# Performance work log

Hardware: AMD Instinct MI355X
Metric: run time of the kernel (lower is better)

The kernel has to match this reference:

```python
import jax, jax.numpy as jnp
import numpy as np

D_MODEL = 2048
D_INNER = 4096   # = d_ssm = nheads * headdim
NHEADS = 64      # = ngroups
DSTATE = 64      # = headdim (d_inner == ngroups * d_state)
D_XB = 1024      # GQA-style shared x/B width
XB_HEADS = D_XB // DSTATE    # 16
REP = NHEADS // XB_HEADS     # repeat_group = 4
DCONV = 4
CHUNK = 128
EPS = 1e-5
BATCH, SEQLEN = 1, 4096
D_IN_PROJ = 2 * D_INNER + 2 * D_XB + NHEADS  # d_mlp == 0
CONV_DIM = D_INNER + 2 * D_XB


def setup_inputs() -> dict:
    key = jax.random.key(0)
    ks = jax.random.split(key, 8)
    u = jax.random.normal(ks[0], (BATCH, SEQLEN, D_MODEL), jnp.float32)
    W_in = jax.random.normal(ks[1], (D_MODEL, D_IN_PROJ), jnp.float32) * np.float32(1.0 / np.sqrt(D_MODEL))
    conv_w = jax.random.uniform(ks[2], (CONV_DIM, DCONV), jnp.float32, -0.5, 0.5)
    conv_b = jnp.zeros((CONV_DIM,), jnp.float32)
    # dt_bias = inverse-softplus of dt sampled log-uniform in [dt_min, dt_max]
    dt = jnp.exp(jax.random.uniform(ks[3], (NHEADS,), jnp.float32) * np.float32(np.log(0.1) - np.log(0.001)) + np.float32(np.log(0.001)))
    dt = jnp.clip(dt, 1e-4, None)
    dt_bias = dt + jnp.log(-jnp.expm1(-dt))
    A_log = jnp.log(jax.random.uniform(ks[4], (NHEADS,), jnp.float32, 1.0, 16.0))
    D = jnp.ones((NHEADS,), jnp.float32)
    norm_weight = jnp.ones((D_INNER,), jnp.float32)
    W_out = jax.random.normal(ks[5], (D_INNER, D_MODEL), jnp.float32) * np.float32(1.0 / np.sqrt(D_INNER))
    return {"u": u, "W_in": W_in, "conv_w": conv_w, "conv_b": conv_b,
            "dt_bias": dt_bias, "A_log": A_log, "D": D,
            "norm_weight": norm_weight, "W_out": W_out}


def _ssd_chunked(x, dt, A, Bm, Cm):
    # x: (b,l,h,p), dt: (b,l,h) post-softplus, A: (h,) negative, Bm/Cm: (b,l,h,n)
    b, l, h, p = x.shape
    n = Bm.shape[-1]
    c, q = l // CHUNK, CHUNK
    rs = lambda t: t.reshape(b, c, q, *t.shape[2:])
    x_c, dt_c, B_c, C_c = rs(x), rs(dt), rs(Bm), rs(Cm)
    dA = dt_c * A                       # (b,c,q,h)
    cum = jnp.cumsum(dA, axis=2)        # (b,c,q,h)
    cumT = jnp.moveaxis(cum, 3, 2)      # (b,c,h,q)
    # intra-chunk: y_i += sum_{j<=i} (C_i.B_j) * exp(cum_i - cum_j) * dt_j * x_j
    diff = cumT[..., :, None] - cumT[..., None, :]               # (b,c,h,q,q)
    M = jnp.where(jnp.tril(jnp.ones((q, q), bool)), jnp.exp(diff), 0.0)
    xdt = x_c * dt_c[..., None]                                  # (b,c,q,h,p)
    G = jnp.einsum('bcihn,bcjhn->bchij', C_c, B_c)
    y = jnp.einsum('bchij,bcjhp->bcihp', G * M, xdt)
    # inter-chunk state passing
    decay_to_end = jnp.exp(cum[:, :, -1:, :] - cum)              # (b,c,q,h)
    S = jnp.einsum('bcjhn,bcjh,bcjhp->bchnp', B_c, decay_to_end, xdt)
    chunk_decay = jnp.exp(cum[:, :, -1, :])                      # (b,c,h)

    def step(H, inp):
        S_c, dec = inp
        return dec[..., None, None] * H + S_c, H

    H0 = jnp.zeros((b, h, n, p), x.dtype)
    _, Hprev = jax.lax.scan(step, H0, (jnp.moveaxis(S, 1, 0), jnp.moveaxis(chunk_decay, 1, 0)))
    Hprev = jnp.moveaxis(Hprev, 0, 1)                            # (b,c,h,n,p)
    y = y + jnp.einsum('bcihn,bcih,bchnp->bcihp', C_c, jnp.exp(cum), Hprev)
    return y.reshape(b, l, h, p)


def reference(u, W_in, conv_w, conv_b, dt_bias, A_log, D, norm_weight, W_out):
    b, l, _ = u.shape
    zxbcdt = u @ W_in                                            # (b,l,D_IN_PROJ)
    z = zxbcdt[..., :D_INNER]
    xBC = zxbcdt[..., D_INNER:D_INNER + CONV_DIM]
    dt = zxbcdt[..., D_INNER + CONV_DIM:]
    # depthwise causal conv1d + SiLU (padding d_conv-1 on the left, output len l)
    xp = jnp.pad(xBC, ((0, 0), (DCONV - 1, 0), (0, 0)))
    conv = conv_b + sum(xp[:, k:k + l, :] * conv_w[:, k] for k in range(DCONV))
    xBC = jax.nn.silu(conv)
    x = xBC[..., :D_XB]
    Bc = xBC[..., D_XB:2 * D_XB]
    Cc = xBC[..., 2 * D_XB:]
    # repeat_kv: (b,l,xb_heads,dstate) -> (b,l,nheads,dstate), interleaved repeats
    x = jnp.repeat(x.reshape(b, l, XB_HEADS, DSTATE), REP, axis=2)
    Bm = jnp.repeat(Bc.reshape(b, l, XB_HEADS, DSTATE), REP, axis=2)
    Cm = Cc.reshape(b, l, NHEADS, DSTATE)
    dt = jax.nn.softplus(dt + dt_bias)                           # dt_softplus=True
    A = -jnp.exp(A_log)
    y = _ssd_chunked(x, dt, A, Bm, Cm) + x * D[:, None]          # per-head D skip
    # gated RMSNorm: group size = d_ssm // ngroups = headdim, norm_before_gate=False
    yz = y * jax.nn.silu(z.reshape(b, l, NHEADS, DSTATE))
    normed = yz * jax.lax.rsqrt(jnp.mean(jnp.square(yz), axis=-1, keepdims=True) + EPS)
    out = normed.reshape(b, l, D_INNER) * norm_weight
    return out @ W_out
```

## Files before the change

kernel.cpp:

```cpp
#include <hip/hip_runtime.h>
#include <hip/hip_bf16.h>
#include <math.h>

typedef __hip_bfloat16 bf16;
typedef __attribute__((ext_vector_type(8))) short short8;
typedef __attribute__((ext_vector_type(4))) float f32x4;

#define D_MODEL   2048
#define D_INNER   4096
#define NHEADS    64
#define DSTATE    64
#define D_XB      1024
#define XB_HEADS  16
#define REP       4
#define DCONV     4
#define CHUNK     128
#define SEQLEN    4096
#define NCHUNK    (SEQLEN / CHUNK)
#define D_IN_PROJ (2*D_INNER + 2*D_XB + NHEADS)
#define NPAD      10496
#define CONV_DIM  (D_INNER + 2*D_XB)
#define EPS       1e-5f
#define LOG2E     1.44269504f

#define Z_BYTES    ((size_t)SEQLEN * D_INNER * 2)
#define RAW_BYTES  ((size_t)SEQLEN * CONV_DIM * 2)
#define DTP_BYTES  ((size_t)SEQLEN * NHEADS * 4)
#define CDEC_BYTES ((size_t)NCHUNK * NHEADS * 4)
#define CONV_BYTES ((size_t)SEQLEN * CONV_DIM * 2)
#define S_BYTES    ((size_t)NCHUNK * NHEADS * DSTATE * DSTATE * 4)
#define U_BYTES    ((size_t)SEQLEN * D_MODEL * 2)
#define RREG_BYTES (CONV_BYTES + S_BYTES)
#define WS_BYTES   (Z_BYTES + RAW_BYTES + DTP_BYTES + CDEC_BYTES + RREG_BYTES)

__device__ __forceinline__ short f2bf(float f) {
  bf16 h = __float2bfloat16(f);
  return *reinterpret_cast<short*>(&h);
}
__device__ __forceinline__ float bf2f(short s) {
  unsigned int u = ((unsigned int)(unsigned short)s) << 16;
  union { unsigned int u; float f; } c; c.u = u; return c.f;
}

__device__ __forceinline__ void gload_lds16(const void* g, void* l) {
  typedef __attribute__((address_space(1))) const unsigned int guint;
  typedef __attribute__((address_space(3))) unsigned int luint;
  __builtin_amdgcn_global_load_lds((guint*)g, (luint*)l, 16, 0, 0);
}

__device__ __forceinline__ char* swz128p(char* b, int r, int c) {
  int o = r * 128 + c * 2; o ^= (r & 7) << 4; return b + o;
}
__device__ __forceinline__ const char* swz128p(const char* b, int r, int c) {
  int o = r * 128 + c * 2; o ^= (r & 7) << 4; return b + o;
}
__device__ __forceinline__ char* swz256p(char* b, int r, int c) {
  int o = r * 256 + c * 2; o ^= (r & 15) << 4; return b + o;
}
__device__ __forceinline__ const char* swz256p(const char* b, int r, int c) {
  int o = r * 256 + c * 2; o ^= (r & 15) << 4; return b + o;
}

__global__ void fill_kernel(float* p, size_t n, float v) {
  size_t i = (size_t)blockIdx.x * blockDim.x + threadIdx.x;
  if (i < n) p[i] = v;
}

__global__ __launch_bounds__(256) void cast_f32_bf16(
    const float* __restrict__ in, short* __restrict__ out, size_t n4) {
  size_t i = (size_t)blockIdx.x * 256 + threadIdx.x;
  if (i >= n4) return;
  float4 v = ((const float4*)in)[i];
  short4 o;
  o.x = f2bf(v.x); o.y = f2bf(v.y); o.z = f2bf(v.z); o.w = f2bf(v.w);
  ((short4*)out)[i] = o;
}

__global__ __launch_bounds__(256) void transpose_cast(
    const float* __restrict__ in, short* __restrict__ out, int R, int C) {
  __shared__ float tile[32][130];
  const int r0 = blockIdx.y * 128;
  const int c0 = blockIdx.x * 32;
  const int tid = threadIdx.x;
  {
    int cq = tid & 7;
    int rbase = tid >> 3;
    bool valid = (c0 + cq * 4) < C;
#pragma unroll
    for (int i = 0; i < 4; ++i) {
      int r = rbase + i * 32;
      float4 v = make_float4(0.f, 0.f, 0.f, 0.f);
      if (valid) v = *(const float4*)(in + (size_t)(r0 + r) * C + c0 + cq * 4);
      tile[cq * 4 + 0][r] = v.x;
      tile[cq * 4 + 1][r] = v.y;
      tile[cq * 4 + 2][r] = v.z;
      tile[cq * 4 + 3][r] = v.w;
    }
  }
  __syncthreads();
  {
    int rq = tid & 31;
    int cbase = tid >> 5;
#pragma unroll
    for (int i = 0; i < 4; ++i) {
      int c = cbase + i * 8;
      short4 o;
      o.x = f2bf(tile[c][rq * 4 + 0]);
      o.y = f2bf(tile[c][rq * 4 + 1]);
      o.z = f2bf(tile[c][rq * 4 + 2]);
      o.w = f2bf(tile[c][rq * 4 + 3]);
      *(short4*)(out + (size_t)(c0 + c) * R + r0 + rq * 4) = o;
    }
  }
}


template<int NLOADS>
__device__ __forceinline__ void stage_half(const char* gtile, int rowbytes,
                                           char* ldst, int tid) {
#pragma unroll
  for (int i = 0; i < NLOADS; ++i) {
    int cid = i * 512 + tid;
    int r = cid >> 2;
    int pos = ((cid & 3) * 16) ^ (((r >> 1) & 3) << 4);
    gload_lds16(gtile + (size_t)r * rowbytes + pos, ldst + cid * 16);
  }
}

template<int BM>
__device__ __forceinline__ void compute_phase(const char* ldsA, const char* ldsB,
    int wm, int wn, int mh, int fr, int kqb, f32x4 (&acc)[BM / 32][4]) {
  constexpr int MF = BM / 64;
  short8 a[MF], b[4];
#pragma unroll
  for (int m = 0; m < MF; ++m) {
    int r = wm * (BM / 2) + mh * (BM / 4) + m * 16 + fr;
    a[m] = *(const short8*)(ldsA + r * 64 + (kqb ^ (((r >> 1) & 3) << 4)));
  }
#pragma unroll
  for (int n = 0; n < 4; ++n) {
    int r = wn * 64 + n * 16 + fr;
    b[n] = *(const short8*)(ldsB + r * 64 + (kqb ^ (((r >> 1) & 3) << 4)));
  }
  __builtin_amdgcn_s_setprio(1);
#pragma unroll
  for (int m = 0; m < MF; ++m)
#pragma unroll
    for (int n = 0; n < 4; ++n)
      acc[mh * MF + m][n] = __builtin_amdgcn_mfma_f32_16x16x32_bf16(a[m], b[n], acc[mh * MF + m][n], 0, 0, 0);
  __builtin_amdgcn_s_setprio(0);
}

template<int N>
__device__ __forceinline__ void wait_bar() {
  if constexpr (N == 0) asm volatile("s_waitcnt vmcnt(0)" ::: "memory");
  else if constexpr (N == 3) asm volatile("s_waitcnt vmcnt(3)" ::: "memory");
  else if constexpr (N == 4) asm volatile("s_waitcnt vmcnt(4)" ::: "memory");
  __builtin_amdgcn_s_barrier();
  __builtin_amdgcn_sched_barrier(0);
}

template<int BM>
__device__ __forceinline__ void gemm_core(const short* A, const short* Bt, int K,
    int rowBase, int colBase, char* lds, f32x4 (&acc)[BM / 32][4]) {
  constexpr int SA = BM * 64;
  constexpr int NLA = SA / 8192;
  constexpr int W = NLA + 2;
  const int tid = threadIdx.x, lane = tid & 63;
  const int w = tid >> 6, wm = w >> 2, wn = w & 3;
  const int fr = lane & 15, kqb = (lane >> 4) * 16;
  const int NT = K >> 6;
  const int rb = K * 2;
  char* ldsA = lds;
  char* ldsB = lds + 4 * SA;
  const char* Ag = (const char*)(A + (size_t)rowBase * K);
  const char* Bg = (const char*)(Bt + (size_t)colBase * K);
  stage_half<NLA>(Ag, rb, ldsA, tid);
  stage_half<2>(Bg, rb, ldsB, tid);
  stage_half<NLA>(Ag + 64, rb, ldsA + SA, tid);
  stage_half<2>(Bg + 64, rb, ldsB + 16384, tid);
  wait_bar<W>();
  for (int t = 0; t < NT; ++t) {
    const int cbA = (t & 1) * 2 * SA, nbA = ((t + 1) & 1) * 2 * SA;
    const int cbB = (t & 1) * 32768, nbB = ((t + 1) & 1) * 32768;
    const size_t ko = (size_t)(t + 1) * 128;
    const bool more = (t + 1 < NT);
    if (more) stage_half<NLA>(Ag + ko, rb, ldsA + nbA, tid);
    compute_phase<BM>(ldsA + cbA, ldsB + cbB, wm, wn, 0, fr, kqb, acc);
    if (more) stage_half<2>(Bg + ko, rb, ldsB + nbB, tid);
    compute_phase<BM>(ldsA + cbA, ldsB + cbB, wm, wn, 1, fr, kqb, acc);
    if (more) { wait_bar<W>(); } else { wait_bar<0>(); }
    if (more) stage_half<NLA>(Ag + ko + 64, rb, ldsA + nbA + SA, tid);
    compute_phase<BM>(ldsA + cbA + SA, ldsB + cbB + 16384, wm, wn, 0, fr, kqb, acc);
    if (more) stage_half<2>(Bg + ko + 64, rb, ldsB + nbB + 16384, tid);
    compute_phase<BM>(ldsA + cbA + SA, ldsB + cbB + 16384, wm, wn, 1, fr, kqb, acc);
    if (more) { wait_bar<W>(); } else { wait_bar<0>(); }
  }
}

__global__ __launch_bounds__(512) void gemm1_8ph(
    const short* __restrict__ A, const short* __restrict__ Bt,
    bf16* __restrict__ z, bf16* __restrict__ raw, float* __restrict__ dtraw) {
  __shared__ __align__(16) char lds[131072];
  f32x4 acc[8][4] = {};
  const int bid = blockIdx.x;
  const int s = (bid & 7) * 82 + (bid >> 3);
  const int rowBase = (s & 15) * 256;
  const int colBase = (s >> 4) * 256;
  gemm_core<256>(A, Bt, D_MODEL, rowBase, colBase, lds, acc);
  const int lane = threadIdx.x & 63, w = threadIdx.x >> 6;
  const int wm = w >> 2, wn = w & 3;
  const int fr = lane & 15, kq = lane >> 4;
  const int r0 = rowBase + wm * 128 + kq * 4;
  const int c0 = colBase + wn * 64 + fr;
#pragma unroll
  for (int M = 0; M < 8; ++M)
#pragma unroll
    for (int n = 0; n < 4; ++n) {
      int col = c0 + n * 16;
#pragma unroll
      for (int j = 0; j < 4; ++j) {
        int row = r0 + M * 16 + j;
        float v = acc[M][n][j];
        if (col < D_INNER) {
          z[(size_t)row * D_INNER + col] = __float2bfloat16(v);
        } else if (col < D_INNER + CONV_DIM) {
          raw[(size_t)row * CONV_DIM + (col - D_INNER)] = __float2bfloat16(v);
        } else if (col < D_IN_PROJ) {
          dtraw[(size_t)row * NHEADS + (col - D_INNER - CONV_DIM)] = v;
        }
      }
    }
}

__global__ __launch_bounds__(512) void gemm2_8ph(
    const short* __restrict__ A, const short* __restrict__ Bt,
    float* __restrict__ C) {
  __shared__ __align__(16) char lds[98304];
  f32x4 acc[4][4] = {};
  const int bid = blockIdx.x;
  const int s = (bid & 7) * 32 + (bid >> 3);
  const int rowBase = (s & 31) * 128;
  const int colBase = (s >> 5) * 256;
  gemm_core<128>(A, Bt, D_INNER, rowBase, colBase, lds, acc);
  const int lane = threadIdx.x & 63, w = threadIdx.x >> 6;
  const int wm = w >> 2, wn = w & 3;
  const int fr = lane & 15, kq = lane >> 4;
  const int r0 = rowBase + wm * 64 + kq * 4;
  const int c0 = colBase + wn * 64 + fr;
#pragma unroll
  for (int M = 0; M < 4; ++M)
#pragma unroll
    for (int n = 0; n < 4; ++n) {
      int col = c0 + n * 16;
#pragma unroll
      for (int j = 0; j < 4; ++j)
        C[(size_t)(r0 + M * 16 + j) * D_MODEL + col] = acc[M][n][j];
    }
}

__global__ __launch_bounds__(256) void conv_silu_kernel(
    const bf16* __restrict__ raw, const float* __restrict__ cw,
    const float* __restrict__ cb, bf16* __restrict__ convout) {
  int idx = blockIdx.x * 256 + threadIdx.x;
  if (idx >= SEQLEN * (CONV_DIM / 8)) return;
  int t = idx / (CONV_DIM / 8);
  int c8 = (idx % (CONV_DIM / 8)) * 8;
  float acc[8];
  float4 w[8];
#pragma unroll
  for (int q = 0; q < 8; ++q) {
    acc[q] = cb[c8 + q];
    w[q] = ((const float4*)cw)[c8 + q];
  }
#pragma unroll
  for (int k = 0; k < DCONV; ++k) {
    int tt = t - (DCONV - 1) + k;
    if (tt < 0) continue;
    short8 v = *(const short8*)((const short*)raw + (size_t)tt * CONV_DIM + c8);
#pragma unroll
    for (int q = 0; q < 8; ++q)
      acc[q] += bf2f(v[q]) * ((const float*)&w[q])[k];
  }
  short8 o;
#pragma unroll
  for (int q = 0; q < 8; ++q) {
    float s = acc[q] / (1.f + expf(-acc[q]));
    o[q] = f2bf(s);
  }
  *(short8*)((short*)convout + (size_t)t * CONV_DIM + c8) = o;
}

__global__ __launch_bounds__(256) void ssd_passA(
    const bf16* __restrict__ conv, const float* __restrict__ dtraw,
    const float* __restrict__ dt_bias, const float* __restrict__ A_log,
    short* __restrict__ Sbuf, float* __restrict__ cdec) {
  __shared__ __align__(16) char sBT[16384];
  __shared__ __align__(16) char sXT[16384];
  __shared__ float sdt[CHUNK], sw[CHUNK], stot[2];
  const int chunk = blockIdx.x, h = blockIdx.y, g = h >> 2;
  const int tid = threadIdx.x, lane = tid & 63, wid = tid >> 6;
  const int t0 = chunk * CHUNK;
  const int fr = lane & 15, kq = lane >> 4;
  short8 rB[4], rX[4];
  {
    const short* cg = (const short*)conv;
#pragma unroll
    for (int it = 0; it < 4; ++it) {
      int cid = tid + it * 256;
      int r = cid >> 3, c8 = (cid & 7) * 8;
      size_t rowoff = (size_t)(t0 + r) * CONV_DIM;
      rB[it] = *(const short8*)(cg + rowoff + D_XB + g * 64 + c8);
      rX[it] = *(const short8*)(cg + rowoff + g * 64 + c8);
    }
    if (tid < CHUNK) {
      float x = dtraw[(size_t)(t0 + tid) * NHEADS + h] + dt_bias[h];
      sdt[tid] = (x > 20.f) ? x : log1pf(expf(x));
    }
  }
  __syncthreads();
  const float Ah2 = -expf(A_log[h]) * LOG2E;
  float s_incl = 0.f;
  if (tid < CHUNK) {
    s_incl = sdt[tid] * Ah2;
#pragma unroll
    for (int off = 1; off < 64; off <<= 1) {
      float tt = __shfl_up(s_incl, off);
      if (lane >= off) s_incl += tt;
    }
    if (lane == 63) stot[wid] = s_incl;
  }
  __syncthreads();
  {
    float s_all = stot[0] + stot[1];
    if (tid < CHUNK) {
      float s = s_incl + ((tid >= 64) ? stot[0] : 0.f);
      sw[tid] = exp2f(s_all - s) * sdt[tid];
    }
    if (tid == 0) cdec[chunk * NHEADS + h] = exp2f(s_all);
  }
  __syncthreads();
#pragma unroll
  for (int it = 0; it < 4; ++it) {
    int cid = tid + it * 256;
    int r = cid >> 3, c8 = (cid & 7) * 8;
    float swr = sw[r];
#pragma unroll
    for (int q = 0; q < 8; ++q) {
      *(short*)swz256p(sBT, c8 + q, r) = rB[it][q];
      *(short*)swz256p(sXT, c8 + q, r) = f2bf(bf2f(rX[it][q]) * swr);
    }
  }
  __syncthreads();
  f32x4 acc[4] = {};
#pragma unroll
  for (int ks = 0; ks < 4; ++ks) {
    short8 a = *(const short8*)swz256p(sXT, wid * 16 + fr, ks * 32 + kq * 8);
    short8 b[4];
#pragma unroll
    for (int n = 0; n < 4; ++n) b[n] = *(const short8*)swz256p(sBT, n * 16 + fr, ks * 32 + kq * 8);
#pragma unroll
    for (int n = 0; n < 4; ++n)
      acc[n] = __builtin_amdgcn_mfma_f32_16x16x32_bf16(a, b[n], acc[n], 0, 0, 0);
  }
  short* So = Sbuf + ((size_t)(chunk * NHEADS + h)) * (DSTATE * DSTATE);
#pragma unroll
  for (int n = 0; n < 4; ++n)
#pragma unroll
    for (int jj = 0; jj < 4; ++jj) {
      int p = wid * 16 + kq * 4 + jj;
      int nc = n * 16 + fr;
      So[p * 64 + nc] = f2bf(acc[n][jj]);
    }
}

__global__ __launch_bounds__(256) void ssd_passB(
    short* __restrict__ Sbuf, const float* __restrict__ cdec) {
  const int h = blockIdx.x;
  const int base = blockIdx.y * 1024 + threadIdx.x * 4;
  float H[4] = {};
  for (int c = 0; c < NCHUNK; ++c) {
    short4* Sc = (short4*)(Sbuf + ((size_t)(c * NHEADS + h)) * (DSTATE * DSTATE) + base);
    short4 v = *Sc;
    short4 o;
    o.x = f2bf(H[0]); o.y = f2bf(H[1]); o.z = f2bf(H[2]); o.w = f2bf(H[3]);
    *Sc = o;
    float dec = cdec[c * NHEADS + h];
    H[0] = dec * H[0] + bf2f(v.x);
    H[1] = dec * H[1] + bf2f(v.y);
    H[2] = dec * H[2] + bf2f(v.z);
    H[3] = dec * H[3] + bf2f(v.w);
  }
}

__global__ __launch_bounds__(256) void ssd_passC(
    const bf16* __restrict__ z, const bf16* __restrict__ conv,
    const float* __restrict__ dtraw, const float* __restrict__ dt_bias,
    const float* __restrict__ A_log, const float* __restrict__ Dv,
    const float* __restrict__ nw, const short* __restrict__ Hprev,
    bf16* __restrict__ normed) {
  __shared__ __align__(16) char sC[16384];
  __shared__ __align__(16) char sBX[16384];
  __shared__ __align__(16) char sP[32768];
  __shared__ __align__(16) char sST[8192];
  __shared__ float sdt[CHUNK], scum2[CHUNK], stot[2];
  const int chunk = blockIdx.x, h = blockIdx.y, g = h >> 2;
  const int tid = threadIdx.x, lane = tid & 63, wid = tid >> 6;
  const int t0 = chunk * CHUNK;
  const int fr = lane & 15, kq = lane >> 4;
  const int wi = wid * 32;
  short8 rX[4];
  {
    const short* cg = (const short*)conv;
#pragma unroll
    for (int it = 0; it < 4; ++it) {
      int cid = tid + it * 256;
      int r = cid >> 3, c8 = (cid & 7) * 8;
      size_t rowoff = (size_t)(t0 + r) * CONV_DIM;
      *(short8*)swz128p(sC, r, c8) = *(const short8*)(cg + rowoff + 2 * D_XB + h * 64 + c8);
      *(short8*)swz128p(sBX, r, c8) = *(const short8*)(cg + rowoff + D_XB + g * 64 + c8);
      rX[it] = *(const short8*)(cg + rowoff + g * 64 + c8);
    }
    if (tid < CHUNK) {
      float x = dtraw[(size_t)(t0 + tid) * NHEADS + h] + dt_bias[h];
      sdt[tid] = (x > 20.f) ? x : log1pf(expf(x));
    }
  }
  __syncthreads();
  const float Ah2 = -expf(A_log[h]) * LOG2E;
  float s_incl = 0.f;
  if (tid < CHUNK) {
    s_incl = sdt[tid] * Ah2;
#pragma unroll
    for (int off = 1; off < 64; off <<= 1) {
      float tt = __shfl_up(s_incl, off);
      if (lane >= off) s_incl += tt;
    }
    if (lane == 63) stot[wid] = s_incl;
  }
  __syncthreads();
  if (tid < CHUNK) scum2[tid] = s_incl + ((tid >= 64) ? stot[0] : 0.f);
  f32x4 accG[2][8] = {};
#pragma unroll
  for (int ks = 0; ks < 2; ++ks) {
    short8 a[2], b[8];
#pragma unroll
    for (int m = 0; m < 2; ++m)
      a[m] = *(const short8*)swz128p(sC, wi + m * 16 + fr, ks * 32 + kq * 8);
#pragma unroll
    for (int n = 0; n < 8; ++n)
      b[n] = *(const short8*)swz128p(sBX, n * 16 + fr, ks * 32 + kq * 8);
#pragma unroll
    for (int m = 0; m < 2; ++m)
#pragma unroll
      for (int n = 0; n < 8; ++n)
        accG[m][n] = __builtin_amdgcn_mfma_f32_16x16x32_bf16(a[m], b[n], accG[m][n], 0, 0, 0);
  }
  __syncthreads();
  {
#pragma unroll
    for (int it = 0; it < 4; ++it) {
      int cid = tid + it * 256;
      int r = cid >> 3, c8 = (cid & 7) * 8;
#pragma unroll
      for (int q = 0; q < 8; ++q)
        *(short*)swz256p(sBX, c8 + q, r) = rX[it][q];
    }
    const short* Hp = Hprev + ((size_t)(chunk * NHEADS + h)) * (DSTATE * DSTATE);
#pragma unroll
    for (int it = 0; it < 2; ++it) {
      int cid = tid + it * 256;
      int pr = cid >> 3, c8 = (cid & 7) * 8;
      *(short8*)swz128p(sST, pr, c8) = *(const short8*)(Hp + pr * 64 + c8);
    }
  }
  __syncthreads();
#pragma unroll
  for (int m = 0; m < 2; ++m)
#pragma unroll
    for (int jj = 0; jj < 4; ++jj) {
      int i = wi + m * 16 + kq * 4 + jj;
      float ci = scum2[i];
#pragma unroll
      for (int n = 0; n < 8; ++n) {
        int j = n * 16 + fr;
        float w = (j <= i) ? exp2f(ci - scum2[j]) * sdt[j] : 0.f;
        *(short*)swz256p(sP, i, j) = f2bf(accG[m][n][jj] * w);
      }
    }
  __syncthreads();
  f32x4 acc1[2][4] = {};
#pragma unroll
  for (int ks = 0; ks < 4; ++ks) {
    short8 a[2], b[4];
#pragma unroll
    for (int m = 0; m < 2; ++m)
      a[m] = *(const short8*)swz256p(sP, wi + m * 16 + fr, ks * 32 + kq * 8);
#pragma unroll
    for (int n = 0; n < 4; ++n)
      b[n] = *(const short8*)swz256p(sBX, n * 16 + fr, ks * 32 + kq * 8);
#pragma unroll
    for (int m = 0; m < 2; ++m)
#pragma unroll
      for (int n = 0; n < 4; ++n)
        acc1[m][n] = __builtin_amdgcn_mfma_f32_16x16x32_bf16(a[m], b[n], acc1[m][n], 0, 0, 0);
  }
  f32x4 acc2[2][4] = {};
#pragma unroll
  for (int ks = 0; ks < 2; ++ks) {
    short8 a[2], b[4];
#pragma unroll
    for (int m = 0; m < 2; ++m)
      a[m] = *(const short8*)swz128p(sC, wi + m * 16 + fr, ks * 32 + kq * 8);
#pragma unroll
    for (int n = 0; n < 4; ++n)
      b[n] = *(const short8*)swz128p(sST, n * 16 + fr, ks * 32 + kq * 8);
#pragma unroll
    for (int m = 0; m < 2; ++m)
#pragma unroll
      for (int n = 0; n < 4; ++n)
        acc2[m][n] = __builtin_amdgcn_mfma_f32_16x16x32_bf16(a[m], b[n], acc2[m][n], 0, 0, 0);
  }
  const float Dh = Dv[h];
#pragma unroll
  for (int m = 0; m < 2; ++m)
#pragma unroll
    for (int jj = 0; jj < 4; ++jj) {
      int i = wi + m * 16 + kq * 4 + jj;
      int t = t0 + i;
      float e2 = exp2f(scum2[i]);
      float vs[4];
      float ss = 0.f;
#pragma unroll
      for (int n = 0; n < 4; ++n) {
        int p = n * 16 + fr;
        float xv = bf2f(((const short*)conv)[(size_t)t * CONV_DIM + g * 64 + p]);
        float zv = bf2f(((const short*)z)[(size_t)t * D_INNER + h * 64 + p]);
        float y = acc1[m][n][jj] + e2 * acc2[m][n][jj] + xv * Dh;
        float sz = zv / (1.f + expf(-zv));
        float v = y * sz;
        vs[n] = v;
        ss += v * v;
      }
      ss += __shfl_xor(ss, 1);
      ss += __shfl_xor(ss, 2);
      ss += __shfl_xor(ss, 4);
      ss += __shfl_xor(ss, 8);
      float rinv = rsqrtf(ss * (1.f / 64.f) + EPS);
#pragma unroll
      for (int n = 0; n < 4; ++n) {
        int p = n * 16 + fr;
        ((short*)normed)[(size_t)t * D_INNER + h * 64 + p] = f2bf(vs[n] * rinv * nw[h * 64 + p]);
      }
    }
}

extern "C" void kernel_launch(void* const* d_in, const int* in_sizes, int n_in,
                              void* d_out, int out_size, void* d_ws, size_t ws_size,
                              hipStream_t stream) {
  const float* u       = (const float*)d_in[0];
  const float* W_in    = (const float*)d_in[1];
  const float* conv_w  = (const float*)d_in[2];
  const float* conv_b  = (const float*)d_in[3];
  const float* dt_bias = (const float*)d_in[4];
  const float* A_log   = (const float*)d_in[5];
  const float* Dv      = (const float*)d_in[6];
  const float* norm_w  = (const float*)d_in[7];
  const float* W_out   = (const float*)d_in[8];
  float* out = (float*)d_out;

  if (ws_size < WS_BYTES) {
    size_t n = (size_t)out_size;
    fill_kernel<<<(n + 255) / 256, 256, 0, stream>>>(out, n, 1000.0f);
    return;
  }

  char* wsb   = (char*)d_ws;
  bf16*  z    = (bf16*)(wsb);
  bf16*  raw  = (bf16*)(wsb + Z_BYTES);
  float* dtp  = (float*)(wsb + Z_BYTES + RAW_BYTES);
  float* cdec = (float*)(wsb + Z_BYTES + RAW_BYTES + DTP_BYTES);
  char*  R    = wsb + Z_BYTES + RAW_BYTES + DTP_BYTES + CDEC_BYTES;
  short* u_bf  = (short*)(R);
  short* WinT  = (short*)(R + U_BYTES);
  bf16*  conv  = (bf16*)(R);
  short* Sbuf  = (short*)(R + CONV_BYTES);
  short* WoutT = (short*)(R);
  bf16*  normed = raw;

  cast_f32_bf16<<<(U_BYTES / 8 + 255) / 256, 256, 0, stream>>>(u, u_bf, U_BYTES / 8);
  {
    dim3 grid(NPAD / 32, D_MODEL / 128);
    transpose_cast<<<grid, 256, 0, stream>>>(W_in, WinT, D_MODEL, D_IN_PROJ);
  }
  gemm1_8ph<<<(NPAD / 256) * (SEQLEN / 256), 512, 0, stream>>>(u_bf, WinT, z, raw, dtp);
  conv_silu_kernel<<<(SEQLEN * (CONV_DIM / 8) + 255) / 256, 256, 0, stream>>>(raw, conv_w, conv_b, conv);
  {
    dim3 grid(NCHUNK, NHEADS);
    ssd_passA<<<grid, 256, 0, stream>>>(conv, dtp, dt_bias, A_log, Sbuf, cdec);
  }
  {
    dim3 grid(NHEADS, 4);
    ssd_passB<<<grid, 256, 0, stream>>>(Sbuf, cdec);
  }
  {
    dim3 grid(NCHUNK, NHEADS);
    ssd_passC<<<grid, 256, 0, stream>>>(z, conv, dtp, dt_bias, A_log, Dv, norm_w, Sbuf, normed);
  }
  {
    dim3 grid(D_MODEL / 32, D_INNER / 128);
    transpose_cast<<<grid, 256, 0, stream>>>(W_out, WoutT, D_INNER, D_MODEL);
  }
  gemm2_8ph<<<(SEQLEN / 128) * (D_MODEL / 256), 512, 0, stream>>>((const short*)normed, WoutT, out);
}
```

Measured before the change: 535.4 us.

## Restructure SSD passC to load C/B/state fragments directly and halve LDS

The intra-chunk SSD kernel now reads the C, B and previous-state MFMA operands straight from global memory into registers instead of staging them in shared memory. It also splits the score matrix into two 64-column halves so the P buffer shrinks to 16KB. Total LDS drops from about 72KB to 32KB, which should allow more blocks per CU and removes several barriers. The cost is uncoalesced, strided global fragment loads (B is read once per wave) and extra wave-local waitcnt/sched barriers between the halves.

```diff
diff --git a/kernel.cpp b/kernel.cpp
--- a/kernel.cpp
+++ b/kernel.cpp
@@ -399,32 +399,25 @@
     const float* __restrict__ A_log, const float* __restrict__ Dv,
     const float* __restrict__ nw, const short* __restrict__ Hprev,
     bf16* __restrict__ normed) {
-  __shared__ __align__(16) char sC[16384];
-  __shared__ __align__(16) char sBX[16384];
-  __shared__ __align__(16) char sP[32768];
-  __shared__ __align__(16) char sST[8192];
+  __shared__ __align__(16) char sXT[16384];
+  __shared__ __align__(16) char sP[16384];
   __shared__ float sdt[CHUNK], scum2[CHUNK], stot[2];
   const int chunk = blockIdx.x, h = blockIdx.y, g = h >> 2;
   const int tid = threadIdx.x, lane = tid & 63, wid = tid >> 6;
   const int t0 = chunk * CHUNK;
   const int fr = lane & 15, kq = lane >> 4;
   const int wi = wid * 32;
+  const short* cg = (const short*)conv;
   short8 rX[4];
-  {
-    const short* cg = (const short*)conv;
-#pragma unroll
-    for (int it = 0; it < 4; ++it) {
-      int cid = tid + it * 256;
-      int r = cid >> 3, c8 = (cid & 7) * 8;
-      size_t rowoff = (size_t)(t0 + r) * CONV_DIM;
-      *(short8*)swz128p(sC, r, c8) = *(const short8*)(cg + rowoff + 2 * D_XB + h * 64 + c8);
-      *(short8*)swz128p(sBX, r, c8) = *(const short8*)(cg + rowoff + D_XB + g * 64 + c8);
-      rX[it] = *(const short8*)(cg + rowoff + g * 64 + c8);
-    }
-    if (tid < CHUNK) {
-      float x = dtraw[(size_t)(t0 + tid) * NHEADS + h] + dt_bias[h];
-      sdt[tid] = (x > 20.f) ? x : log1pf(expf(x));
-    }
+#pragma unroll
+  for (int it = 0; it < 4; ++it) {
+    int cid = tid + it * 256;
+    int r = cid >> 3, c8 = (cid & 7) * 8;
+    rX[it] = *(const short8*)(cg + (size_t)(t0 + r) * CONV_DIM + g * 64 + c8);
+  }
+  if (tid < CHUNK) {
+    float x = dtraw[(size_t)(t0 + tid) * NHEADS + h] + dt_bias[h];
+    sdt[tid] = (x > 20.f) ? x : log1pf(expf(x));
   }
   __syncthreads();
   const float Ah2 = -expf(A_log[h]) * LOG2E;
@@ -438,88 +431,91 @@
     }
     if (lane == 63) stot[wid] = s_incl;
   }
+#pragma unroll
+  for (int it = 0; it < 4; ++it) {
+    int cid = tid + it * 256;
+    int r = cid >> 3, c8 = (cid & 7) * 8;
+#pragma unroll
+    for (int q = 0; q < 8; ++q)
+      *(short*)swz256p(sXT, c8 + q, r) = rX[it][q];
+  }
   __syncthreads();
   if (tid < CHUNK) scum2[tid] = s_incl + ((tid >= 64) ? stot[0] : 0.f);
-  f32x4 accG[2][8] = {};
-#pragma unroll
-  for (int ks = 0; ks < 2; ++ks) {
-    short8 a[2], b[8];
+  short8 aC[2][2];
+#pragma unroll
+  for (int ks = 0; ks < 2; ++ks)
 #pragma unroll
     for (int m = 0; m < 2; ++m)
-      a[m] = *(const short8*)swz128p(sC, wi + m * 16 + fr, ks * 32 + kq * 8);
-#pragma unroll
-    for (int n = 0; n < 8; ++n)
-      b[n] = *(const short8*)swz128p(sBX, n * 16 + fr, ks * 32 + kq * 8);
+      aC[ks][m] = *(const short8*)(cg + (size_t)(t0 + wi + m * 16 + fr) * CONV_DIM
+                                   + 2 * D_XB + h * 64 + ks * 32 + kq * 8);
+  __syncthreads();
+  f32x4 acc1[2][4] = {};
+#pragma unroll
+  for (int half = 0; half < 2; ++half) {
+    f32x4 accG[2][4] = {};
+#pragma unroll
+    for (int ks = 0; ks < 2; ++ks) {
+      short8 b[4];
+#pragma unroll
+      for (int n = 0; n < 4; ++n) {
+        int j = half * 64 + n * 16 + fr;
+        b[n] = *(const short8*)(cg + (size_t)(t0 + j) * CONV_DIM + D_XB + g * 64 + ks * 32 + kq * 8);
+      }
+#pragma unroll
+      for (int m = 0; m < 2; ++m)
+#pragma unroll
+        for (int n = 0; n < 4; ++n)
+          accG[m][n] = __builtin_amdgcn_mfma_f32_16x16x32_bf16(aC[ks][m], b[n], accG[m][n], 0, 0, 0);
+    }
 #pragma unroll
     for (int m = 0; m < 2; ++m)
 #pragma unroll
-      for (int n = 0; n < 8; ++n)
-        accG[m][n] = __builtin_amdgcn_mfma_f32_16x16x32_bf16(a[m], b[n], accG[m][n], 0, 0, 0);
-  }
-  __syncthreads();
-  {
-#pragma unroll
-    for (int it = 0; it < 4; ++it) {
-      int cid = tid + it * 256;
-      int r = cid >> 3, c8 = (cid & 7) * 8;
-#pragma unroll
-      for (int q = 0; q < 8; ++q)
-        *(short*)swz256p(sBX, c8 + q, r) = rX[it][q];
-    }
+      for (int jj = 0; jj < 4; ++jj) {
+        int i = wi + m * 16 + kq * 4 + jj;
+        float ci = scum2[i];
+#pragma unroll
+        for (int n = 0; n < 4; ++n) {
+          int j = half * 64 + n * 16 + fr;
+          float w = (j <= i) ? exp2f(ci - scum2[j]) * sdt[j] : 0.f;
+          *(short*)swz128p(sP, i, n * 16 + fr) = f2bf(accG[m][n][jj] * w);
+        }
+      }
+    asm volatile("s_waitcnt lgkmcnt(0)" ::: "memory");
+    __builtin_amdgcn_sched_barrier(0);
+#pragma unroll
+    for (int ks2 = 0; ks2 < 2; ++ks2) {
+      int ko = half * 64 + ks2 * 32 + kq * 8;
+      short8 a[2], b[4];
+#pragma unroll
+      for (int m = 0; m < 2; ++m)
+        a[m] = *(const short8*)swz128p(sP, wi + m * 16 + fr, ks2 * 32 + kq * 8);
+#pragma unroll
+      for (int n = 0; n < 4; ++n)
+        b[n] = *(const short8*)swz256p(sXT, n * 16 + fr, ko);
+#pragma unroll
+      for (int m = 0; m < 2; ++m)
+#pragma unroll
+        for (int n = 0; n < 4; ++n)
+          acc1[m][n] = __builtin_amdgcn_mfma_f32_16x16x32_bf16(a[m], b[n], acc1[m][n], 0, 0, 0);
+    }
+    asm volatile("s_waitcnt lgkmcnt(0)" ::: "memory");
+    __builtin_amdgcn_sched_barrier(0);
+  }
+  f32x4 acc2[2][4] = {};
+  {
     const short* Hp = Hprev + ((size_t)(chunk * NHEADS + h)) * (DSTATE * DSTATE);
 #pragma unroll
-    for (int it = 0; it < 2; ++it) {
-      int cid = tid + it * 256;
-      int pr = cid >> 3, c8 = (cid & 7) * 8;
-      *(short8*)swz128p(sST, pr, c8) = *(const short8*)(Hp + pr * 64 + c8);
-    }
-  }
-  __syncthreads();
-#pragma unroll
-  for (int m = 0; m < 2; ++m)
-#pragma unroll
-    for (int jj = 0; jj < 4; ++jj) {
-      int i = wi + m * 16 + kq * 4 + jj;
-      float ci = scum2[i];
-#pragma unroll
-      for (int n = 0; n < 8; ++n) {
-        int j = n * 16 + fr;
-        float w = (j <= i) ? exp2f(ci - scum2[j]) * sdt[j] : 0.f;
-        *(short*)swz256p(sP, i, j) = f2bf(accG[m][n][jj] * w);
-      }
-    }
-  __syncthreads();
-  f32x4 acc1[2][4] = {};
-#pragma unroll
-  for (int ks = 0; ks < 4; ++ks) {
-    short8 a[2], b[4];
-#pragma unroll
-    for (int m = 0; m < 2; ++m)
-      a[m] = *(const short8*)swz256p(sP, wi + m * 16 + fr, ks * 32 + kq * 8);
-#pragma unroll
-    for (int n = 0; n < 4; ++n)
-      b[n] = *(const short8*)swz256p(sBX, n * 16 + fr, ks * 32 + kq * 8);
-#pragma unroll
-    for (int m = 0; m < 2; ++m)
+    for (int ks = 0; ks < 2; ++ks) {
+      short8 b[4];
 #pragma unroll
       for (int n = 0; n < 4; ++n)
-        acc1[m][n] = __builtin_amdgcn_mfma_f32_16x16x32_bf16(a[m], b[n], acc1[m][n], 0, 0, 0);
-  }
-  f32x4 acc2[2][4] = {};
-#pragma unroll
-  for (int ks = 0; ks < 2; ++ks) {
-    short8 a[2], b[4];
-#pragma unroll
-    for (int m = 0; m < 2; ++m)
-      a[m] = *(const short8*)swz128p(sC, wi + m * 16 + fr, ks * 32 + kq * 8);
-#pragma unroll
-    for (int n = 0; n < 4; ++n)
-      b[n] = *(const short8*)swz128p(sST, n * 16 + fr, ks * 32 + kq * 8);
-#pragma unroll
-    for (int m = 0; m < 2; ++m)
-#pragma unroll
-      for (int n = 0; n < 4; ++n)
-        acc2[m][n] = __builtin_amdgcn_mfma_f32_16x16x32_bf16(a[m], b[n], acc2[m][n], 0, 0, 0);
+        b[n] = *(const short8*)(Hp + (n * 16 + fr) * 64 + ks * 32 + kq * 8);
+#pragma unroll
+      for (int m = 0; m < 2; ++m)
+#pragma unroll
+        for (int n = 0; n < 4; ++n)
+          acc2[m][n] = __builtin_amdgcn_mfma_f32_16x16x32_bf16(aC[ks][m], b[n], acc2[m][n], 0, 0, 0);
+    }
   }
   const float Dh = Dv[h];
 #pragma unroll
@@ -534,7 +530,7 @@
 #pragma unroll
       for (int n = 0; n < 4; ++n) {
         int p = n * 16 + fr;
-        float xv = bf2f(((const short*)conv)[(size_t)t * CONV_DIM + g * 64 + p]);
+        float xv = bf2f(cg[(size_t)t * CONV_DIM + g * 64 + p]);
         float zv = bf2f(((const short*)z)[(size_t)t * D_INNER + h * 64 + p]);
         float y = acc1[m][n][jj] + e2 * acc2[m][n][jj] + xv * Dh;
         float sz = zv / (1.f + expf(-zv));
```

Result: no change. 539.1 us (+0.7%).
